# Kernel optimization log

Hardware: AMD Instinct MI355X
Metric: run time of the kernel (lower is better)

The kernel has to match this reference:

```python
import jax, jax.numpy as jnp
import numpy as np
from jax import lax

DECAY = 0.99
EPS = 1e-5
K = 2048   # n_embeddings
D = 256    # embedding_dim
B, T = 32, 1024


def setup_inputs() -> dict:
    key = jax.random.key(0)
    k1, k2 = jax.random.split(key)
    z_e = jax.random.normal(k1, (B, T, D), dtype=jnp.float32)
    embedding = jax.random.normal(k2, (K, D), dtype=jnp.float32)
    ema_count = jnp.zeros((K,), dtype=jnp.float32)
    ema_weight = embedding
    return {"z_e": z_e, "embedding": embedding, "ema_count": ema_count, "ema_weight": ema_weight}


def reference(z_e, embedding, ema_count, ema_weight):
    Bb, Tt, Dd = z_e.shape
    Kk = embedding.shape[0]
    flat = z_e.reshape(-1, Dd)                                   # [N, D], N = B*T
    dist = (jnp.sum(flat * flat, axis=1, keepdims=True)
            - 2.0 * flat @ embedding.T
            + jnp.sum(embedding * embedding, axis=1))            # [N, K]
    indices = jnp.argmin(dist, axis=1)                           # [N] int
    z_q = embedding[indices].reshape(Bb, Tt, Dd)                 # gather

    # --- EMA codebook update (training branch, no_grad in torch) ---
    ones = jnp.ones_like(indices, dtype=flat.dtype)
    new_count = jax.ops.segment_sum(ones, indices, num_segments=Kk)      # [K]
    ema_count_new = ema_count * DECAY + (1.0 - DECAY) * new_count
    total = jnp.sum(ema_count_new)
    ema_count_new = (ema_count_new + EPS) / (total + Kk * EPS) * total   # Laplace smoothing
    new_weight = jax.ops.segment_sum(flat, indices, num_segments=Kk)     # [K, D] scatter-add
    ema_weight_new = ema_weight * DECAY + (1.0 - DECAY) * new_weight
    embedding_new = ema_weight_new / ema_count_new[:, None]

    codebook_loss = jnp.mean(jnp.square(lax.stop_gradient(z_e) - z_q))
    commitment_loss = jnp.mean(jnp.square(z_e - lax.stop_gradient(z_q)))
    z_q_st = z_e + lax.stop_gradient(z_q - z_e)                  # straight-through
    return (z_q_st, indices.reshape(Bb, Tt), codebook_loss, commitment_loss,
            embedding_new, ema_count_new, ema_weight_new)
```

## Files before the change

### kernel.cpp

```cpp
#include <hip/hip_runtime.h>


#define DECAY 0.99f
#define OMD   0.01f
#define EPSC  1e-5f
#define MARGIN 0.025f

constexpr int Dq = 256;
constexpr int Kn = 2048;
constexpr int Nq = 32768;
constexpr int MAXITEMS = 3072;

typedef short bf16x8 __attribute__((ext_vector_type(8)));
typedef float f32x4 __attribute__((ext_vector_type(4)));

__device__ __forceinline__ unsigned short f2bf_rne(float f) {
    unsigned int u = __float_as_uint(f);
    unsigned int r = u + 0x7FFFu + ((u >> 16) & 1u);
    return (unsigned short)(r >> 16);
}
__device__ __forceinline__ float bf2f(unsigned short h) {
    return __uint_as_float(((unsigned int)h) << 16);
}
__device__ __forceinline__ void async_copy16(const void* g, void* l) {
    __builtin_amdgcn_global_load_lds(
        (const __attribute__((address_space(1))) unsigned int*)g,
        (__attribute__((address_space(3))) unsigned int*)l, 16, 0, 0);
}
__device__ __forceinline__ uint4 packbf(const unsigned short* h) {
    uint4 u;
    u.x = (unsigned)h[0] | ((unsigned)h[1] << 16);
    u.y = (unsigned)h[2] | ((unsigned)h[3] << 16);
    u.z = (unsigned)h[4] | ((unsigned)h[5] << 16);
    u.w = (unsigned)h[6] | ((unsigned)h[7] << 16);
    return u;
}

__global__ __launch_bounds__(256) void convert_kernel(
    const float* __restrict__ x, const float* __restrict__ emb,
    unsigned char* __restrict__ xh_g, unsigned char* __restrict__ xl_g,
    unsigned char* __restrict__ eh_g, unsigned char* __restrict__ el_g,
    float* __restrict__ enorm, int* __restrict__ counts,
    float* __restrict__ loss_acc, int* __restrict__ nflagF,
    int* __restrict__ nitems, int* __restrict__ nflagP)
{
    __shared__ float part[32][8];
    int b = blockIdx.x;
    bool is_e = (b >= 1024);
    const float* src = is_e ? emb : x;
    unsigned char* hg = is_e ? eh_g : xh_g;
    unsigned char* lg = is_e ? el_g : xl_g;
    int base_row = (is_e ? (b - 1024) : b) * 32;
    int t = threadIdx.x;
    if (b == 1024) {
        for (int i = t; i < Kn; i += 256) counts[i] = 0;
        if (t == 0) { loss_acc[0] = 0.f; nflagF[0] = 0; nitems[0] = 0; nflagP[0] = 0; }
    }
    int rg = t >> 7, ds = (t >> 4) & 7, rl = t & 15;
    int r = base_row + rg * 16 + rl;
    const float4* s4 = (const float4*)(src + (size_t)r * Dq + ds * 32);
    float v[32];
#pragma unroll
    for (int i = 0; i < 8; ++i) {
        float4 f = s4[i];
        v[i * 4 + 0] = f.x; v[i * 4 + 1] = f.y; v[i * 4 + 2] = f.z; v[i * 4 + 3] = f.w;
    }
    unsigned short hh[32], ll[32];
#pragma unroll
    for (int i = 0; i < 32; ++i) {
        hh[i] = f2bf_rne(v[i]);
        ll[i] = f2bf_rne(v[i] - bf2f(hh[i]));
    }
    size_t gb = ((size_t)(r >> 4) * 8 + ds) * 1024 + rl * 16;
#pragma unroll
    for (int qd = 0; qd < 4; ++qd) {
        *(uint4*)(hg + gb + qd * 256) = packbf(hh + qd * 8);
        *(uint4*)(lg + gb + qd * 256) = packbf(ll + qd * 8);
    }
    if (is_e) {
        float ps = 0.f;
#pragma unroll
        for (int i = 0; i < 32; ++i) ps += v[i] * v[i];
        part[rg * 16 + rl][ds] = ps;
        __syncthreads();
        if (t < 32) {
            float s = 0.f;
#pragma unroll
            for (int j = 0; j < 8; ++j) s += part[t][j];
            enorm[base_row + t] = s;
        }
    }
}

__global__ __launch_bounds__(256, 2) void argmin_kernel(
    const unsigned char* __restrict__ xh_g, const unsigned char* __restrict__ xl_g,
    const unsigned char* __restrict__ eh_g, const unsigned char* __restrict__ el_g,
    const float* __restrict__ enorm,
    float* __restrict__ ws_s1, float* __restrict__ ws_s2,
    float* __restrict__ ws_s3, int* __restrict__ ws_ik)
{
    __shared__ __align__(16) unsigned char lds[69632];
    const int tid = threadIdx.x;
    const int lane = tid & 63, wave = tid >> 6;
    const int wq = wave >> 1, wk = wave & 1;
    const int rl = lane & 15, quad = lane >> 4;
    const int b = blockIdx.x;
    const int qb = (b & 7) * 32 + ((b >> 3) >> 1);
    const int split = (b >> 3) & 1;
    const int lane16 = lane * 16;

    auto STAGE = [&](int s) {
        const int kt = s >> 3, ch = s & 7;
        unsigned char* buf = lds + (s & 1) * 32768;
        const unsigned char* src = (wave == 0) ? xh_g : (wave == 1) ? xl_g
                                  : (wave == 2) ? eh_g : el_g;
        const int rb = (wave < 2) ? qb * 8 : (split * 64 + kt * 8);
#pragma unroll
        for (int jj = 0; jj < 8; ++jj)
            async_copy16(src + ((size_t)(rb + jj) * 8 + ch) * 1024 + lane16,
                         buf + wave * 8192 + jj * 1024);
    };

    ((float4*)(lds + 65536))[tid] = ((const float4*)(enorm + split * 1024))[tid];
    STAGE(0);
    __syncthreads();

    float s1[16], s2[16], s3[16];
    int i1[16], i2[16];
#pragma unroll
    for (int s = 0; s < 16; ++s) {
        s1[s] = 3.4e38f; s2[s] = 3.4e38f; s3[s] = 3.4e38f; i1[s] = 0; i2[s] = 0;
    }
    f32x4 acc[4][4];

    for (int s = 0; s < 64; ++s) {
        const int kt = s >> 3, ch = s & 7;
        if (ch == 0) {
#pragma unroll
            for (int mf = 0; mf < 4; ++mf)
#pragma unroll
                for (int nf = 0; nf < 4; ++nf)
                    acc[mf][nf] = (f32x4){0.f, 0.f, 0.f, 0.f};
        }
        if (s < 63) STAGE(s + 1);

        const unsigned char* buf = lds + (s & 1) * 32768;
        bf16x8 ah[4], al[4], bh[4], bl[4];
#pragma unroll
        for (int mf = 0; mf < 4; ++mf) {
            ah[mf] = *(const bf16x8*)(buf + (wq * 4 + mf) * 1024 + lane16);
            al[mf] = *(const bf16x8*)(buf + 8192 + (wq * 4 + mf) * 1024 + lane16);
        }
#pragma unroll
        for (int nf = 0; nf < 4; ++nf) {
            bh[nf] = *(const bf16x8*)(buf + 16384 + (wk * 4 + nf) * 1024 + lane16);
            bl[nf] = *(const bf16x8*)(buf + 24576 + (wk * 4 + nf) * 1024 + lane16);
        }
#pragma unroll
        for (int mf = 0; mf < 4; ++mf)
#pragma unroll
            for (int nf = 0; nf < 4; ++nf) {
                acc[mf][nf] = __builtin_amdgcn_mfma_f32_16x16x32_bf16(
                    ah[mf], bh[nf], acc[mf][nf], 0, 0, 0);
                acc[mf][nf] = __builtin_amdgcn_mfma_f32_16x16x32_bf16(
                    ah[mf], bl[nf], acc[mf][nf], 0, 0, 0);
                acc[mf][nf] = __builtin_amdgcn_mfma_f32_16x16x32_bf16(
                    al[mf], bh[nf], acc[mf][nf], 0, 0, 0);
            }

        if (ch == 7) {
#pragma unroll
            for (int nf = 0; nf < 4; ++nf) {
                float ee = *(const float*)(lds + 65536 +
                             (kt * 128 + wk * 64 + nf * 16 + rl) * 4);
                int code = kt * 4 + nf;
#pragma unroll
                for (int mf = 0; mf < 4; ++mf)
#pragma unroll
                    for (int r = 0; r < 4; ++r) {
                        int slot = mf * 4 + r;
                        float sc = fmaf(-2.f, acc[mf][nf][r], ee);
                        bool lt1 = sc < s1[slot];
                        bool lt2 = sc < s2[slot];
                        s3[slot] = lt2 ? s2[slot] : fminf(s3[slot], sc);
                        s2[slot] = lt1 ? s1[slot] : (lt2 ? sc : s2[slot]);
                        i2[slot] = lt1 ? i1[slot] : (lt2 ? code : i2[slot]);
                        s1[slot] = lt1 ? sc : s1[slot];
                        i1[slot] = lt1 ? code : i1[slot];
                    }
            }
        }
        __syncthreads();
    }

    int k1[16], k2[16];
#pragma unroll
    for (int s = 0; s < 16; ++s) {
        k1[s] = split * 1024 + (i1[s] >> 2) * 128 + wk * 64 + (i1[s] & 3) * 16 + rl;
        k2[s] = split * 1024 + (i2[s] >> 2) * 128 + wk * 64 + (i2[s] & 3) * 16 + rl;
    }
#pragma unroll
    for (int m = 1; m <= 8; m <<= 1) {
#pragma unroll
        for (int s = 0; s < 16; ++s) {
            float t1 = __shfl_xor(s1[s], m, 64);
            float t2 = __shfl_xor(s2[s], m, 64);
            float t3 = __shfl_xor(s3[s], m, 64);
            int   j1 = __shfl_xor(k1[s], m, 64);
            int   j2 = __shfl_xor(k2[s], m, 64);
            bool a1 = (t1 < s1[s]) || (t1 == s1[s] && j1 < k1[s]);
            bool a2 = (t1 < s2[s]) || (t1 == s2[s] && j1 < k2[s]);
            s3[s] = a2 ? s2[s] : fminf(s3[s], t1);
            s2[s] = a1 ? s1[s] : (a2 ? t1 : s2[s]);
            k2[s] = a1 ? k1[s] : (a2 ? j1 : k2[s]);
            s1[s] = a1 ? t1 : s1[s];
            k1[s] = a1 ? j1 : k1[s];
            bool b1 = (t2 < s1[s]) || (t2 == s1[s] && j2 < k1[s]);
            bool b2 = (t2 < s2[s]) || (t2 == s2[s] && j2 < k2[s]);
            s3[s] = b2 ? s2[s] : fminf(s3[s], t2);
            s2[s] = b1 ? s1[s] : (b2 ? t2 : s2[s]);
            k2[s] = b1 ? k1[s] : (b2 ? j2 : k2[s]);
            s1[s] = b1 ? t2 : s1[s];
            k1[s] = b1 ? j2 : k1[s];
            s3[s] = fminf(s3[s], t3);
        }
    }
    __syncthreads();
    float* rs1 = (float*)lds;
    float* rs2 = (float*)(lds + 1024);
    float* rs3 = (float*)(lds + 2048);
    int*   rk  = (int*)(lds + 3072);
    if (rl == 0) {
#pragma unroll
        for (int s = 0; s < 16; ++s) {
            int ql = wq * 64 + (s >> 2) * 16 + quad * 4 + (s & 3);
            rs1[ql * 2 + wk] = s1[s];
            rs2[ql * 2 + wk] = s2[s];
            rs3[ql * 2 + wk] = s3[s];
            rk[ql * 2 + wk]  = k1[s] | (k2[s] << 11);
        }
    }
    __syncthreads();
    if (tid < 128) {
        float a1 = rs1[tid * 2], a2 = rs2[tid * 2], a3 = rs3[tid * 2];
        int kk = rk[tid * 2];
        int m1 = kk & 2047, m2 = (kk >> 11) & 2047;
        float t1 = rs1[tid * 2 + 1], t2 = rs2[tid * 2 + 1], t3 = rs3[tid * 2 + 1];
        int kj = rk[tid * 2 + 1];
        int j1 = kj & 2047, j2 = (kj >> 11) & 2047;
        bool c1 = (t1 < a1) || (t1 == a1 && j1 < m1);
        bool c2 = (t1 < a2) || (t1 == a2 && j1 < m2);
        a3 = c2 ? a2 : fminf(a3, t1);
        a2 = c1 ? a1 : (c2 ? t1 : a2);
        m2 = c1 ? m1 : (c2 ? j1 : m2);
        a1 = c1 ? t1 : a1;
        m1 = c1 ? j1 : m1;
        bool d1 = (t2 < a1) || (t2 == a1 && j2 < m1);
        bool d2 = (t2 < a2) || (t2 == a2 && j2 < m2);
        a3 = d2 ? a2 : fminf(a3, t2);
        a2 = d1 ? a1 : (d2 ? t2 : a2);
        m2 = d1 ? m1 : (d2 ? j2 : m2);
        a1 = d1 ? t2 : a1;
        m1 = d1 ? j2 : m1;
        a3 = fminf(a3, t3);
        int q = qb * 128 + tid;
        ws_s1[split * Nq + q] = a1;
        ws_s2[split * Nq + q] = a2;
        ws_s3[split * Nq + q] = a3;
        ws_ik[split * Nq + q] = m1 | (m2 << 11);
    }
}

__global__ __launch_bounds__(256) void pick_kernel(
    const float* __restrict__ ws_s1, const float* __restrict__ ws_s2,
    const float* __restrict__ ws_s3, const int* __restrict__ ws_ik,
    int* __restrict__ idx,
    int* __restrict__ nflagF, int* __restrict__ flaglist,
    int* __restrict__ nflagP, int* __restrict__ pairlist)
{
    int q = blockIdx.x * 256 + threadIdx.x;
    float a1 = ws_s1[q], a2 = ws_s2[q], a3 = ws_s3[q];
    int kk = ws_ik[q];
    int m1 = kk & 2047, m2 = (kk >> 11) & 2047;
    float t1 = ws_s1[Nq + q], t2 = ws_s2[Nq + q], t3 = ws_s3[Nq + q];
    int kj = ws_ik[Nq + q];
    int j1 = kj & 2047, j2 = (kj >> 11) & 2047;
    bool c1 = (t1 < a1) || (t1 == a1 && j1 < m1);
    bool c2 = (t1 < a2) || (t1 == a2 && j1 < m2);
    a3 = c2 ? a2 : fminf(a3, t1);
    a2 = c1 ? a1 : (c2 ? t1 : a2);
    m2 = c1 ? m1 : (c2 ? j1 : m2);
    a1 = c1 ? t1 : a1;
    m1 = c1 ? j1 : m1;
    bool d1 = (t2 < a1) || (t2 == a1 && j2 < m1);
    bool d2 = (t2 < a2) || (t2 == a2 && j2 < m2);
    a3 = d2 ? a2 : fminf(a3, t2);
    a2 = d1 ? a1 : (d2 ? t2 : a2);
    m2 = d1 ? m1 : (d2 ? j2 : m2);
    a1 = d1 ? t2 : a1;
    m1 = d1 ? j2 : m1;
    a3 = fminf(a3, t3);

    idx[q] = m1;
    if (a3 - a1 < MARGIN) {
        int p = atomicAdd(nflagF, 1);
        flaglist[p] = q;
    } else if (a2 - a1 < MARGIN) {
        int p = atomicAdd(nflagP, 1);
        pairlist[p] = q | (m2 << 16);
    }
}

__global__ __launch_bounds__(256) void rescue_kernel(
    const float* __restrict__ x, const float* __restrict__ emb,
    const float* __restrict__ enorm, const int* __restrict__ flaglist,
    const int* __restrict__ nflag, int* __restrict__ idx)
{
    __shared__ float xs[256];
    __shared__ float bsc[256];
    __shared__ int bix[256];
    int nf = nflag[0];
    int t = threadIdx.x;
    for (int it = blockIdx.x; it < nf; it += gridDim.x) {
        __syncthreads();
        int q = flaglist[it];
        xs[t] = x[(size_t)q * Dq + t];
        __syncthreads();
        float best = 3.4e38f;
        int bk = 0;
        for (int j = 0; j < 8; ++j) {
            int k = j * 256 + t;
            const float4* e4 = (const float4*)(emb + (size_t)k * Dq);
            const float4* x4 = (const float4*)xs;
            float d = 0.f;
#pragma unroll 8
            for (int c = 0; c < 64; ++c) {
                float4 e = e4[c], xv = x4[c];
                d = fmaf(e.x, xv.x, d); d = fmaf(e.y, xv.y, d);
                d = fmaf(e.z, xv.z, d); d = fmaf(e.w, xv.w, d);
            }
            float sc = enorm[k] - 2.f * d;
            if (sc < best || (sc == best && k < bk)) { best = sc; bk = k; }
        }
        bsc[t] = best; bix[t] = bk;
        __syncthreads();
        for (int o = 128; o > 0; o >>= 1) {
            if (t < o) {
                float so = bsc[t + o]; int io = bix[t + o];
                if (so < bsc[t] || (so == bsc[t] && io < bix[t])) {
                    bsc[t] = so; bix[t] = io;
                }
            }
            __syncthreads();
        }
        if (t == 0) idx[q] = bix[0];
    }
}

__global__ __launch_bounds__(256) void rescue_pair_kernel(
    const float* __restrict__ x, const float* __restrict__ emb,
    const float* __restrict__ enorm, const int* __restrict__ pairlist,
    const int* __restrict__ nflagP, int* __restrict__ idx)
{
    int np = nflagP[0];
    for (int p = blockIdx.x * 256 + threadIdx.x; p < np; p += gridDim.x * 256) {
        int e = pairlist[p];
        int q = e & 0xFFFF;
        int c2 = e >> 16;
        int c1 = idx[q];
        const float4* x4 = (const float4*)(x + (size_t)q * Dq);
        const float4* e1 = (const float4*)(emb + (size_t)c1 * Dq);
        const float4* e2 = (const float4*)(emb + (size_t)c2 * Dq);
        float d1 = 0.f, d2 = 0.f;
#pragma unroll 8
        for (int c = 0; c < 64; ++c) {
            float4 xv = x4[c];
            float4 ea = e1[c];
            float4 eb = e2[c];
            d1 = fmaf(ea.x, xv.x, d1); d1 = fmaf(ea.y, xv.y, d1);
            d1 = fmaf(ea.z, xv.z, d1); d1 = fmaf(ea.w, xv.w, d1);
            d2 = fmaf(eb.x, xv.x, d2); d2 = fmaf(eb.y, xv.y, d2);
            d2 = fmaf(eb.z, xv.z, d2); d2 = fmaf(eb.w, xv.w, d2);
        }
        float sc1 = enorm[c1] - 2.f * d1;
        float sc2 = enorm[c2] - 2.f * d2;
        if (sc2 < sc1 || (sc2 == sc1 && c2 < c1)) idx[q] = c2;
    }
}

__global__ __launch_bounds__(256) void hist_kernel(const int* __restrict__ idx,
                                                   int* __restrict__ counts) {
    int q = blockIdx.x * 256 + threadIdx.x;
    atomicAdd(&counts[idx[q]], 1);
}

__global__ __launch_bounds__(256) void scan_kernel(
    const int* __restrict__ counts, const float* __restrict__ ema_count,
    int* __restrict__ offs, int* __restrict__ cursor,
    float* __restrict__ cnew, float* __restrict__ out_count,
    int* __restrict__ items, int* __restrict__ nitems)
{
    __shared__ int   si[256];
    __shared__ float sf[256];
    int t = threadIdx.x;
    int c[8], pre[8];
    int run = 0;
    float se = 0.f;
#pragma unroll
    for (int i = 0; i < 8; ++i) {
        c[i] = counts[t * 8 + i];
        pre[i] = run;
        run += c[i];
        se += ema_count[t * 8 + i];
    }
    si[t] = run;
    sf[t] = se;
    __syncthreads();
    for (int off = 1; off < 256; off <<= 1) {
        int v = (t >= off) ? si[t - off] : 0;
        __syncthreads();
        si[t] += v;
        __syncthreads();
    }
    int total_n = si[255];
    int base = si[t] - run;
    for (int off = 128; off > 0; off >>= 1) {
        if (t < off) sf[t] += sf[t + off];
        __syncthreads();
    }
    float total = DECAY * sf[0] + OMD * (float)total_n;
    float denom = total + 2048.0f * EPSC;
#pragma unroll
    for (int i = 0; i < 8; ++i) {
        int k = t * 8 + i;
        int o = base + pre[i];
        offs[k] = o;
        cursor[k] = o;
        float ck = DECAY * ema_count[k] + OMD * (float)c[i];
        float v = (ck + EPSC) / denom * total;
        cnew[k] = v;
        out_count[k] = v;
        if (c[i] > 0) {
            int nit = (c[i] + 31) >> 5;
            int ib = atomicAdd(nitems, nit);
            for (int j = 0; j < nit; ++j)
                items[ib + j] = (k << 17) | (o + j * 32);
        }
    }
}

__global__ __launch_bounds__(256) void fill_kernel(const int* __restrict__ idx,
                                                   int* __restrict__ cursor,
                                                   int* __restrict__ sorted) {
    int n = blockIdx.x * 256 + threadIdx.x;
    int v = idx[n];
    int pos = atomicAdd(&cursor[v], 1);
    sorted[pos] = n;
}

__global__ __launch_bounds__(256) void weight_partial_kernel(
    const float* __restrict__ x, const int* __restrict__ sorted,
    const int* __restrict__ items, const int* __restrict__ nitems,
    const int* __restrict__ counts, const int* __restrict__ offs,
    float* __restrict__ accum)
{
    if ((int)blockIdx.x >= nitems[0]) return;
    int it = items[blockIdx.x];
    int k = it >> 17;
    int start = it & 0x1FFFF;
    int end = min(start + 32, offs[k] + counts[k]);
    int t = threadIdx.x;
    float acc = 0.f;
    int j = start;
    for (; j + 4 <= end; j += 4) {
        int n0 = sorted[j + 0], n1 = sorted[j + 1];
        int n2 = sorted[j + 2], n3 = sorted[j + 3];
        float v0 = x[(size_t)n0 * Dq + t];
        float v1 = x[(size_t)n1 * Dq + t];
        float v2 = x[(size_t)n2 * Dq + t];
        float v3 = x[(size_t)n3 * Dq + t];
        acc += v0 + v1 + v2 + v3;
    }
    for (; j < end; ++j) {
        int n = sorted[j];
        acc += x[(size_t)n * Dq + t];
    }
    atomicAdd(&accum[(size_t)k * Dq + t], acc);
}

__global__ __launch_bounds__(256) void weight_final_kernel(
    const float* __restrict__ accum, const float* __restrict__ ema_weight,
    const float* __restrict__ cnew,
    float* __restrict__ out_embed, float* __restrict__ out_weight)
{
    int gi = blockIdx.x * 256 + threadIdx.x;
    int k = gi >> 6;
    float4 a = ((const float4*)accum)[gi];
    float4 ew = ((const float4*)ema_weight)[gi];
    float inv = 1.f / cnew[k];
    float4 w;
    w.x = DECAY * ew.x + OMD * a.x;
    w.y = DECAY * ew.y + OMD * a.y;
    w.z = DECAY * ew.z + OMD * a.z;
    w.w = DECAY * ew.w + OMD * a.w;
    ((float4*)out_weight)[gi] = w;
    float4 e;
    e.x = w.x * inv; e.y = w.y * inv; e.z = w.z * inv; e.w = w.w * inv;
    ((float4*)out_embed)[gi] = e;
}

__global__ __launch_bounds__(256) void finalize_kernel(
    const int* __restrict__ idx, const float* __restrict__ x,
    const float* __restrict__ emb, float* __restrict__ idx_f_out,
    float* __restrict__ zq_out, float* __restrict__ loss_acc)
{
    __shared__ int sidx[64];
    __shared__ float lpart[4];
    const int tid = threadIdx.x;
    const int q0 = blockIdx.x * 64;
    if (tid < 64) {
        int b = idx[q0 + tid];
        idx_f_out[q0 + tid] = (float)b;
        sidx[tid] = b;
    }
    __syncthreads();
    int gq = tid >> 2, part = tid & 3;
    int bk = sidx[gq];
    const float4* ev = (const float4*)&emb[(size_t)bk * Dq + part * 64];
    const float4* xv = (const float4*)&x[(size_t)(q0 + gq) * Dq + part * 64];
    float4* ov = (float4*)&zq_out[(size_t)(q0 + gq) * Dq + part * 64];
    float lacc = 0.f;
#pragma unroll 4
    for (int t2 = 0; t2 < 16; ++t2) {
        float4 e4 = ev[t2];
        float4 x4 = xv[t2];
        ov[t2] = e4;
        float d0 = x4.x - e4.x, d1 = x4.y - e4.y;
        float d2 = x4.z - e4.z, d3 = x4.w - e4.w;
        lacc += d0 * d0 + d1 * d1 + d2 * d2 + d3 * d3;
    }
#pragma unroll
    for (int o = 32; o > 0; o >>= 1) lacc += __shfl_down(lacc, o, 64);
    if ((tid & 63) == 0) lpart[tid >> 6] = lacc;
    __syncthreads();
    if (tid == 0)
        atomicAdd(loss_acc, lpart[0] + lpart[1] + lpart[2] + lpart[3]);
}

__global__ void loss_final_kernel(const float* __restrict__ loss_acc,
                                  float* __restrict__ out_cb,
                                  float* __restrict__ out_cm) {
    float v = loss_acc[0] / (float)((size_t)Nq * Dq);
    out_cb[0] = v;
    out_cm[0] = v;
}

extern "C" void kernel_launch(void* const* d_in, const int* in_sizes, int n_in,
                              void* d_out, int out_size, void* d_ws, size_t ws_size,
                              hipStream_t stream) {
    const float* z_e        = (const float*)d_in[0];
    const float* emb        = (const float*)d_in[1];
    const float* ema_count  = (const float*)d_in[2];
    const float* ema_weight = (const float*)d_in[3];

    float* out_zq     = (float*)d_out;
    float* out_idx    = out_zq + (size_t)Nq * Dq;
    float* out_cb     = out_idx + Nq;
    float* out_cm     = out_cb + 1;
    float* out_embed  = out_cm + 1;
    float* out_count  = out_embed + (size_t)Kn * Dq;
    float* out_weight = out_count + Kn;

    unsigned char* xh_g = (unsigned char*)d_out;
    unsigned char* xl_g = xh_g + 16777216;
    size_t eh_off = (((size_t)8421378 * 4) + 15) & ~(size_t)15;
    unsigned char* eh_g = (unsigned char*)d_out + eh_off;
    unsigned char* el_g = eh_g + 1048576;
    float* accum = (float*)d_out;

    char* ws = (char*)d_ws;
    float* enorm    = (float*)(ws + 0);
    int*   counts   = (int*)(ws + 8192);
    int*   offs     = (int*)(ws + 16384);
    int*   cursor   = (int*)(ws + 24576);
    float* cnew     = (float*)(ws + 32768);
    float* loss_acc = (float*)(ws + 40960);
    int*   nflagF   = (int*)(ws + 40964);
    int*   nitems   = (int*)(ws + 40968);
    int*   nflagP   = (int*)(ws + 40972);
    int*   idx      = (int*)(ws + 49152);
    int*   sorted   = (int*)(ws + 180224);
    int*   flaglist = (int*)(ws + 311296);
    float* ws_s1    = (float*)(ws + 442368);
    float* ws_s2    = (float*)(ws + 704512);
    float* ws_s3    = (float*)(ws + 966656);
    int*   ws_ik    = (int*)(ws + 1228800);
    int*   pairlist = (int*)(ws + 1490944);
    int*   items    = (int*)(ws + 1622016);

    convert_kernel<<<1088, 256, 0, stream>>>(z_e, emb, xh_g, xl_g, eh_g, el_g,
                                             enorm, counts, loss_acc, nflagF,
                                             nitems, nflagP);
    argmin_kernel<<<512, 256, 0, stream>>>(xh_g, xl_g, eh_g, el_g, enorm,
                                           ws_s1, ws_s2, ws_s3, ws_ik);
    hipMemsetAsync(accum, 0, (size_t)Kn * Dq * sizeof(float), stream);
    pick_kernel<<<Nq / 256, 256, 0, stream>>>(ws_s1, ws_s2, ws_s3, ws_ik, idx,
                                              nflagF, flaglist, nflagP, pairlist);
    rescue_kernel<<<1024, 256, 0, stream>>>(z_e, emb, enorm, flaglist, nflagF, idx);
    rescue_pair_kernel<<<128, 256, 0, stream>>>(z_e, emb, enorm, pairlist,
                                                nflagP, idx);
    hist_kernel<<<Nq / 256, 256, 0, stream>>>(idx, counts);
    scan_kernel<<<1, 256, 0, stream>>>(counts, ema_count, offs, cursor, cnew,
                                       out_count, items, nitems);
    fill_kernel<<<Nq / 256, 256, 0, stream>>>(idx, cursor, sorted);
    weight_partial_kernel<<<MAXITEMS, 256, 0, stream>>>(z_e, sorted, items, nitems,
                                                        counts, offs, accum);
    weight_final_kernel<<<Kn * Dq / 1024, 256, 0, stream>>>(accum, ema_weight, cnew,
                                                            out_embed, out_weight);
    finalize_kernel<<<Nq / 64, 256, 0, stream>>>(idx, z_e, emb, out_idx,
                                                 out_zq, loss_acc);
    loss_final_kernel<<<1, 1, 0, stream>>>(loss_acc, out_cb, out_cm);
}
```

Baseline: 322.2 us.

## Enlarge argmin tile to 512 threads with async triple-buffered codebook pipeline

```diff
diff --git a/kernel.cpp b/kernel.cpp
--- a/kernel.cpp
+++ b/kernel.cpp
@@ -92,37 +92,52 @@
     }
 }
 
-__global__ __launch_bounds__(256, 2) void argmin_kernel(
+__global__ __launch_bounds__(512, 2) void argmin_kernel(
     const unsigned char* __restrict__ xh_g, const unsigned char* __restrict__ xl_g,
     const unsigned char* __restrict__ eh_g, const unsigned char* __restrict__ el_g,
     const float* __restrict__ enorm,
     float* __restrict__ ws_s1, float* __restrict__ ws_s2,
     float* __restrict__ ws_s3, int* __restrict__ ws_ik)
 {
-    __shared__ __align__(16) unsigned char lds[69632];
+    __shared__ __align__(16) unsigned char lds[118784];
     const int tid = threadIdx.x;
     const int lane = tid & 63, wave = tid >> 6;
     const int wq = wave >> 1, wk = wave & 1;
     const int rl = lane & 15, quad = lane >> 4;
     const int b = blockIdx.x;
-    const int qb = (b & 7) * 32 + ((b >> 3) >> 1);
+    const int qb = (b & 7) * 16 + (b >> 4);
     const int split = (b >> 3) & 1;
     const int lane16 = lane * 16;
 
-    auto STAGE = [&](int s) {
-        const int kt = s >> 3, ch = s & 7;
-        unsigned char* buf = lds + (s & 1) * 32768;
-        const unsigned char* src = (wave == 0) ? xh_g : (wave == 1) ? xl_g
-                                  : (wave == 2) ? eh_g : el_g;
-        const int rb = (wave < 2) ? qb * 8 : (split * 64 + kt * 8);
+    auto STAGE_X = [&](int s2) {
+        const int ch = s2 & 7;
+        unsigned char* dst = lds + (s2 & 1) * 32768 + ((wave < 2) ? 0 : 16384);
+        const unsigned char* src = (wave < 2) ? xh_g : xl_g;
+        const int jj0 = (wave & 1) * 8;
 #pragma unroll
         for (int jj = 0; jj < 8; ++jj)
-            async_copy16(src + ((size_t)(rb + jj) * 8 + ch) * 1024 + lane16,
-                         buf + wave * 8192 + jj * 1024);
+            async_copy16(src + ((size_t)(qb * 16 + jj0 + jj) * 8 + ch) * 1024 + lane16,
+                         dst + (jj0 + jj) * 1024);
     };
-
-    ((float4*)(lds + 65536))[tid] = ((const float4*)(enorm + split * 1024))[tid];
-    STAGE(0);
+    auto STAGE_E = [&](int s2) {
+        const int kt = s2 >> 3, ch = s2 & 7;
+        unsigned char* dst = lds + 65536 + (s2 % 3) * 16384 + ((wave < 6) ? 0 : 8192);
+        const unsigned char* src = (wave < 6) ? eh_g : el_g;
+        const int jj0 = (wave & 1) * 4;
+#pragma unroll
+        for (int jj = 0; jj < 4; ++jj)
+            async_copy16(src + ((size_t)(split * 64 + kt * 8 + jj0 + jj) * 8 + ch) * 1024
+                             + lane16,
+                         dst + (jj0 + jj) * 1024);
+    };
+
+    ((float2*)(lds + 114688))[tid] = ((const float2*)(enorm + split * 1024))[tid];
+    if (wave < 4) {
+        STAGE_X(0);
+    } else {
+        STAGE_E(0);
+        STAGE_E(1);
+    }
     __syncthreads();
 
     float s1[16], s2[16], s3[16];
@@ -142,20 +157,30 @@
                 for (int nf = 0; nf < 4; ++nf)
                     acc[mf][nf] = (f32x4){0.f, 0.f, 0.f, 0.f};
         }
-        if (s < 63) STAGE(s + 1);
-
-        const unsigned char* buf = lds + (s & 1) * 32768;
+        if (wave < 4) {
+            if (s + 1 < 64) STAGE_X(s + 1);
+        } else {
+            if (s + 2 < 64) STAGE_E(s + 2);
+        }
+        if (s < 62)      asm volatile("s_waitcnt vmcnt(8)" ::: "memory");
+        else if (s == 62) asm volatile("s_waitcnt vmcnt(4)" ::: "memory");
+        else             asm volatile("s_waitcnt vmcnt(0)" ::: "memory");
+        __builtin_amdgcn_s_barrier();
+
+        const unsigned char* xb = lds + (s & 1) * 32768;
+        const unsigned char* eb = lds + 65536 + (s % 3) * 16384;
         bf16x8 ah[4], al[4], bh[4], bl[4];
 #pragma unroll
         for (int mf = 0; mf < 4; ++mf) {
-            ah[mf] = *(const bf16x8*)(buf + (wq * 4 + mf) * 1024 + lane16);
-            al[mf] = *(const bf16x8*)(buf + 8192 + (wq * 4 + mf) * 1024 + lane16);
+            ah[mf] = *(const bf16x8*)(xb + (wq * 4 + mf) * 1024 + lane16);
+            al[mf] = *(const bf16x8*)(xb + 16384 + (wq * 4 + mf) * 1024 + lane16);
         }
 #pragma unroll
         for (int nf = 0; nf < 4; ++nf) {
-            bh[nf] = *(const bf16x8*)(buf + 16384 + (wk * 4 + nf) * 1024 + lane16);
-            bl[nf] = *(const bf16x8*)(buf + 24576 + (wk * 4 + nf) * 1024 + lane16);
-        }
+            bh[nf] = *(const bf16x8*)(eb + (wk * 4 + nf) * 1024 + lane16);
+            bl[nf] = *(const bf16x8*)(eb + 8192 + (wk * 4 + nf) * 1024 + lane16);
+        }
+        __builtin_amdgcn_s_setprio(1);
 #pragma unroll
         for (int mf = 0; mf < 4; ++mf)
 #pragma unroll
@@ -167,11 +192,12 @@
                 acc[mf][nf] = __builtin_amdgcn_mfma_f32_16x16x32_bf16(
                     al[mf], bh[nf], acc[mf][nf], 0, 0, 0);
             }
+        __builtin_amdgcn_s_setprio(0);
 
         if (ch == 7) {
 #pragma unroll
             for (int nf = 0; nf < 4; ++nf) {
-                float ee = *(const float*)(lds + 65536 +
+                float ee = *(const float*)(lds + 114688 +
                              (kt * 128 + wk * 64 + nf * 16 + rl) * 4);
                 int code = kt * 4 + nf;
 #pragma unroll
@@ -190,7 +216,6 @@
                     }
             }
         }
-        __syncthreads();
     }
 
     int k1[16], k2[16];
@@ -227,9 +252,9 @@
     }
     __syncthreads();
     float* rs1 = (float*)lds;
-    float* rs2 = (float*)(lds + 1024);
-    float* rs3 = (float*)(lds + 2048);
-    int*   rk  = (int*)(lds + 3072);
+    float* rs2 = (float*)(lds + 2048);
+    float* rs3 = (float*)(lds + 4096);
+    int*   rk  = (int*)(lds + 6144);
     if (rl == 0) {
 #pragma unroll
         for (int s = 0; s < 16; ++s) {
@@ -241,7 +266,7 @@
         }
     }
     __syncthreads();
-    if (tid < 128) {
+    if (tid < 256) {
         float a1 = rs1[tid * 2], a2 = rs2[tid * 2], a3 = rs3[tid * 2];
         int kk = rk[tid * 2];
         int m1 = kk & 2047, m2 = (kk >> 11) & 2047;
@@ -263,7 +288,7 @@
         a1 = d1 ? t2 : a1;
         m1 = d1 ? j2 : m1;
         a3 = fminf(a3, t3);
-        int q = qb * 128 + tid;
+        int q = qb * 256 + tid;
         ws_s1[split * Nq + q] = a1;
         ws_s2[split * Nq + q] = a2;
         ws_s3[split * Nq + q] = a3;
@@ -601,7 +626,7 @@
     convert_kernel<<<1088, 256, 0, stream>>>(z_e, emb, xh_g, xl_g, eh_g, el_g,
                                              enorm, counts, loss_acc, nflagF,
                                              nitems, nflagP);
-    argmin_kernel<<<512, 256, 0, stream>>>(xh_g, xl_g, eh_g, el_g, enorm,
+    argmin_kernel<<<256, 512, 0, stream>>>(xh_g, xl_g, eh_g, el_g, enorm,
                                            ws_s1, ws_s2, ws_s3, ws_ik);
     hipMemsetAsync(accum, 0, (size_t)Kn * Dq * sizeof(float), stream);
     pick_kernel<<<Nq / 256, 256, 0, stream>>>(ws_s1, ws_s2, ws_s3, ws_ik, idx,
```

Measured after the change: 332.1 us. 3.1% more time.

## Fuse histogram, memset, rescue passes and final kernels to cut launches

Applied to the files above, without the earlier changes.

```diff
diff --git a/kernel.cpp b/kernel.cpp
--- a/kernel.cpp
+++ b/kernel.cpp
@@ -276,9 +276,16 @@
     const float* __restrict__ ws_s3, const int* __restrict__ ws_ik,
     int* __restrict__ idx,
     int* __restrict__ nflagF, int* __restrict__ flaglist,
-    int* __restrict__ nflagP, int* __restrict__ pairlist)
+    int* __restrict__ nflagP, int* __restrict__ pairlist,
+    int* __restrict__ counts, float* __restrict__ accum)
 {
-    int q = blockIdx.x * 256 + threadIdx.x;
+    int b = blockIdx.x;
+    if (b >= 128) {
+        int zi = (b - 128) * 256 + threadIdx.x;
+        ((float4*)accum)[zi] = (float4){0.f, 0.f, 0.f, 0.f};
+        return;
+    }
+    int q = b * 256 + threadIdx.x;
     float a1 = ws_s1[q], a2 = ws_s2[q], a3 = ws_s3[q];
     int kk = ws_ik[q];
     int m1 = kk & 2047, m2 = (kk >> 11) & 2047;
@@ -302,6 +309,7 @@
     a3 = fminf(a3, t3);
 
     idx[q] = m1;
+    atomicAdd(&counts[m1], 1);
     if (a3 - a1 < MARGIN) {
         int p = atomicAdd(nflagF, 1);
         flaglist[p] = q;
@@ -314,13 +322,15 @@
 __global__ __launch_bounds__(256) void rescue_kernel(
     const float* __restrict__ x, const float* __restrict__ emb,
     const float* __restrict__ enorm, const int* __restrict__ flaglist,
-    const int* __restrict__ nflag, int* __restrict__ idx)
+    const int* __restrict__ nflagF, const int* __restrict__ pairlist,
+    const int* __restrict__ nflagP, int* __restrict__ idx,
+    int* __restrict__ counts)
 {
     __shared__ float xs[256];
     __shared__ float bsc[256];
     __shared__ int bix[256];
-    int nf = nflag[0];
-    int t = threadIdx.x;
+    const int t = threadIdx.x;
+    int nf = nflagF[0];
     for (int it = blockIdx.x; it < nf; it += gridDim.x) {
         __syncthreads();
         int q = flaglist[it];
@@ -353,17 +363,17 @@
             }
             __syncthreads();
         }
-        if (t == 0) idx[q] = bix[0];
-    }
-}
-
-__global__ __launch_bounds__(256) void rescue_pair_kernel(
-    const float* __restrict__ x, const float* __restrict__ emb,
-    const float* __restrict__ enorm, const int* __restrict__ pairlist,
-    const int* __restrict__ nflagP, int* __restrict__ idx)
-{
+        if (t == 0) {
+            int old = idx[q];
+            if (bix[0] != old) {
+                idx[q] = bix[0];
+                atomicSub(&counts[old], 1);
+                atomicAdd(&counts[bix[0]], 1);
+            }
+        }
+    }
     int np = nflagP[0];
-    for (int p = blockIdx.x * 256 + threadIdx.x; p < np; p += gridDim.x * 256) {
+    for (int p = blockIdx.x * 256 + t; p < np; p += gridDim.x * 256) {
         int e = pairlist[p];
         int q = e & 0xFFFF;
         int c2 = e >> 16;
@@ -384,14 +394,12 @@
         }
         float sc1 = enorm[c1] - 2.f * d1;
         float sc2 = enorm[c2] - 2.f * d2;
-        if (sc2 < sc1 || (sc2 == sc1 && c2 < c1)) idx[q] = c2;
-    }
-}
-
-__global__ __launch_bounds__(256) void hist_kernel(const int* __restrict__ idx,
-                                                   int* __restrict__ counts) {
-    int q = blockIdx.x * 256 + threadIdx.x;
-    atomicAdd(&counts[idx[q]], 1);
+        if (sc2 < sc1 || (sc2 == sc1 && c2 < c1)) {
+            idx[q] = c2;
+            atomicSub(&counts[c1], 1);
+            atomicAdd(&counts[c2], 1);
+        }
+    }
 }
 
 __global__ __launch_bounds__(256) void scan_kernel(
@@ -488,28 +496,10 @@
     atomicAdd(&accum[(size_t)k * Dq + t], acc);
 }
 
-__global__ __launch_bounds__(256) void weight_final_kernel(
+__global__ __launch_bounds__(256) void wf_fin_kernel(
     const float* __restrict__ accum, const float* __restrict__ ema_weight,
     const float* __restrict__ cnew,
-    float* __restrict__ out_embed, float* __restrict__ out_weight)
-{
-    int gi = blockIdx.x * 256 + threadIdx.x;
-    int k = gi >> 6;
-    float4 a = ((const float4*)accum)[gi];
-    float4 ew = ((const float4*)ema_weight)[gi];
-    float inv = 1.f / cnew[k];
-    float4 w;
-    w.x = DECAY * ew.x + OMD * a.x;
-    w.y = DECAY * ew.y + OMD * a.y;
-    w.z = DECAY * ew.z + OMD * a.z;
-    w.w = DECAY * ew.w + OMD * a.w;
-    ((float4*)out_weight)[gi] = w;
-    float4 e;
-    e.x = w.x * inv; e.y = w.y * inv; e.z = w.z * inv; e.w = w.w * inv;
-    ((float4*)out_embed)[gi] = e;
-}
-
-__global__ __launch_bounds__(256) void finalize_kernel(
+    float* __restrict__ out_embed, float* __restrict__ out_weight,
     const int* __restrict__ idx, const float* __restrict__ x,
     const float* __restrict__ emb, float* __restrict__ idx_f_out,
     float* __restrict__ zq_out, float* __restrict__ loss_acc)
@@ -517,11 +507,29 @@
     __shared__ int sidx[64];
     __shared__ float lpart[4];
     const int tid = threadIdx.x;
-    const int q0 = blockIdx.x * 64;
+    const int b = blockIdx.x;
+    if (b < 512) {
+        int gi = b * 256 + tid;
+        int k = gi >> 6;
+        float4 a = ((const float4*)accum)[gi];
+        float4 ew = ((const float4*)ema_weight)[gi];
+        float inv = 1.f / cnew[k];
+        float4 w;
+        w.x = DECAY * ew.x + OMD * a.x;
+        w.y = DECAY * ew.y + OMD * a.y;
+        w.z = DECAY * ew.z + OMD * a.z;
+        w.w = DECAY * ew.w + OMD * a.w;
+        ((float4*)out_weight)[gi] = w;
+        float4 e;
+        e.x = w.x * inv; e.y = w.y * inv; e.z = w.z * inv; e.w = w.w * inv;
+        ((float4*)out_embed)[gi] = e;
+        return;
+    }
+    const int q0 = (b - 512) * 64;
     if (tid < 64) {
-        int b = idx[q0 + tid];
-        idx_f_out[q0 + tid] = (float)b;
-        sidx[tid] = b;
+        int bi = idx[q0 + tid];
+        idx_f_out[q0 + tid] = (float)bi;
+        sidx[tid] = bi;
     }
     __syncthreads();
     int gq = tid >> 2, part = tid & 3;
@@ -603,21 +611,19 @@
                                              nitems, nflagP);
     argmin_kernel<<<512, 256, 0, stream>>>(xh_g, xl_g, eh_g, el_g, enorm,
                                            ws_s1, ws_s2, ws_s3, ws_ik);
-    hipMemsetAsync(accum, 0, (size_t)Kn * Dq * sizeof(float), stream);
-    pick_kernel<<<Nq / 256, 256, 0, stream>>>(ws_s1, ws_s2, ws_s3, ws_ik, idx,
-                                              nflagF, flaglist, nflagP, pairlist);
-    rescue_kernel<<<1024, 256, 0, stream>>>(z_e, emb, enorm, flaglist, nflagF, idx);
-    rescue_pair_kernel<<<128, 256, 0, stream>>>(z_e, emb, enorm, pairlist,
-                                                nflagP, idx);
-    hist_kernel<<<Nq / 256, 256, 0, stream>>>(idx, counts);
+    pick_kernel<<<640, 256, 0, stream>>>(ws_s1, ws_s2, ws_s3, ws_ik, idx,
+                                         nflagF, flaglist, nflagP, pairlist,
+                                         counts, accum);
+    rescue_kernel<<<1024, 256, 0, stream>>>(z_e, emb, enorm, flaglist, nflagF,
+                                            pairlist, nflagP, idx, counts);
     scan_kernel<<<1, 256, 0, stream>>>(counts, ema_count, offs, cursor, cnew,
                                        out_count, items, nitems);
     fill_kernel<<<Nq / 256, 256, 0, stream>>>(idx, cursor, sorted);
     weight_partial_kernel<<<MAXITEMS, 256, 0, stream>>>(z_e, sorted, items, nitems,
                                                         counts, offs, accum);
-    weight_final_kernel<<<Kn * Dq / 1024, 256, 0, stream>>>(accum, ema_weight, cnew,
-                                                            out_embed, out_weight);
-    finalize_kernel<<<Nq / 64, 256, 0, stream>>>(idx, z_e, emb, out_idx,
-                                                 out_zq, loss_acc);
+    wf_fin_kernel<<<1024, 256, 0, stream>>>(accum, ema_weight, cnew,
+                                            out_embed, out_weight,
+                                            idx, z_e, emb, out_idx,
+                                            out_zq, loss_acc);
     loss_final_kernel<<<1, 1, 0, stream>>>(loss_acc, out_cb, out_cm);
 }
```

Measured after the change: 320.0 us. No clear change (-0.7%).
